# Kernel tuning notes

Hardware: AMD Instinct MI355X
Metric: run time of the kernel (lower is better)

The kernel has to match this reference:

```python
import jax, jax.numpy as jnp
import numpy as np

# Algorithm constants (scaled-down but structure-identical to the source:
# original Nxy=2304, Nz=300, ItN=60, ROISize=300, NxyExt=128, BkgMean=110, SNR=200)
ItN = 2
BkgMean = 110.0
ROISize = 256
SNR = 200.0
NxyExt = 64
Nxy = 1024
Nz = 24
LO = Nxy // 2 - ROISize   # ROI start inside the padded FFT plane
HI = Nxy // 2 + ROISize   # ROI end


def setup_inputs() -> dict:
    key = jax.random.key(0)
    k1, k2, k3, k4 = jax.random.split(key, 4)
    # raw camera image; uniform in [0, 400) so that subtracting BkgMean=110 keeps signal
    imstack = jax.random.uniform(k1, (1, 1, Nxy - 2 * NxyExt, Nxy - 2 * NxyExt), dtype=jnp.float32) * 400.0
    # initial object volume estimate (the `init` ctor arg)
    init_vol = jax.random.uniform(k2, (1, Nz, 2 * ROISize, 2 * ROISize), dtype=jnp.float32)
    # learned frequency-domain PSF kernel (rand * 0.001, as in __init__)
    conv_real = jax.random.uniform(k3, (1, 1, Nxy, Nxy), dtype=jnp.float32) * 0.001
    conv_imag = jax.random.uniform(k4, (1, 1, Nxy, Nxy), dtype=jnp.float32) * 0.001
    return {"imstack": imstack, "init_vol": init_vol, "conv_real": conv_real, "conv_imag": conv_imag}


def reference(imstack, init_vol, conv_real, conv_imag):
    # Complex frequency-domain kernel; constant across iterations (the source
    # rebuilds/casts it every slice -- same math, hoisted here).
    K = (conv_real + 1j * conv_imag)[0, 0]            # [Nxy, Nxy] complex
    Ksum = jnp.sum(conv_real)

    img = jnp.maximum(imstack - BkgMean, 0.0)
    ImgExp = jnp.pad(img, ((0, 0), (0, 0), (NxyExt, NxyExt), (NxyExt, NxyExt)))  # [1,1,Nxy,Nxy]

    obj = init_vol                                     # [1, Nz, 2R, 2R]
    for _ in range(ItN):
        # --- forward projection: batched over all Nz slices (source loops) ---
        # each slice is placed into the center ROI of a zero [Nxy,Nxy] plane
        vol = jnp.pad(obj, ((0, 0), (0, 0), (LO, Nxy - HI), (LO, Nxy - HI)))  # [1,Nz,Nxy,Nxy]
        est = jnp.real(jnp.fft.ifft2(jnp.fft.fft2(vol) * K)) / Ksum
        ImgEst = jnp.sum(jnp.maximum(est, 0.0), axis=1, keepdims=True)        # [1,1,Nxy,Nxy]

        # --- ratio image (interior only; border stays 1) ---
        Tmp = jnp.median(ImgEst)
        inner = ImgExp[:, :, NxyExt:-NxyExt, NxyExt:-NxyExt] / (
            ImgEst[:, :, NxyExt:-NxyExt, NxyExt:-NxyExt] + Tmp / SNR)
        Ratio = jnp.ones((1, 1, Nxy, Nxy), dtype=ImgEst.dtype)
        Ratio = Ratio.at[:, :, NxyExt:-NxyExt, NxyExt:-NxyExt].set(inner)

        # --- back projection: in the source, fft2(Ratio)*conj(K) is identical for
        # every jj (Ratio and K do not change inside the loop), so compute once ---
        back = jnp.real(jnp.fft.ifft2(jnp.fft.fft2(Ratio) * jnp.conj(K))) / Ksum
        back = jnp.maximum(back, 0.0)                  # [1,1,Nxy,Nxy]
        obj = obj * back[:, :, LO:HI, LO:HI]           # broadcast over Nz
    return obj
```

## Files before the change

### kernel.cpp

```cpp
#include <hip/hip_runtime.h>
#include <math.h>

#define NXY  1024
#define NZ   24
#define ROI2 512
#define LO_  256
#define EXT  64
#define IMGW 896
#define ITN  2
#define SNR_ 200.0f
#define BKG  110.0f
#define RANK1 524287u
#define RANK2 524288u
#define NACC 4
#define SWZ(i) ((i) ^ ((((i) >> 4) & 3) * 5))

typedef float2 cf;

__device__ __forceinline__ cf cadd(cf a, cf b) { return make_float2(a.x + b.x, a.y + b.y); }
__device__ __forceinline__ cf csub(cf a, cf b) { return make_float2(a.x - b.x, a.y - b.y); }
__device__ __forceinline__ cf cmul(cf a, cf b) { return make_float2(a.x * b.x - a.y * b.y, a.x * b.y + a.y * b.x); }

struct Tw { const cf *t0, *t1, *t2, *t3; };

__device__ __forceinline__ void twinit_all(cf* TW0, cf* T1, cf* T2, cf* T3) {
  const float W = -6.28318530717958647692f / 1024.0f;
  int k = threadIdx.x;
  float s, c;
  sincosf(W * (float)k, &s, &c);
  TW0[k] = make_float2(c, s);
  if (k < 64) { sincosf(W * (float)(4 * k), &s, &c);  T1[k] = make_float2(c, s); }
  if (k < 16) { sincosf(W * (float)(16 * k), &s, &c); T2[k] = make_float2(c, s); }
  if (k < 4)  { sincosf(W * (float)(64 * k), &s, &c); T3[k] = make_float2(c, s); }
}

template <int SIGN, int T0>
__device__ cf* fft1024_r4_t(cf* src, cf* dst, Tw tw) {
  const int tid = threadIdx.x;
#pragma unroll
  for (int t = T0; t < 5; ++t) {
    __syncthreads();
    const int s = 1 << (2 * t);
    const int q = tid & (s - 1);
    cf a0 = src[SWZ(tid)];
    cf a1 = src[SWZ(tid + 256)];
    cf a2 = src[SWZ(tid + 512)];
    cf a3 = src[SWZ(tid + 768)];
    cf b0 = cadd(a0, a2), b1 = csub(a0, a2);
    cf b2 = cadd(a1, a3), b3 = csub(a1, a3);
    cf jb3 = (SIGN < 0) ? make_float2(b3.y, -b3.x) : make_float2(-b3.y, b3.x);
    cf c0 = cadd(b0, b2);
    cf c2 = csub(b0, b2);
    cf c1 = cadd(b1, jb3);
    cf c3 = csub(b1, jb3);
    const int base = 4 * tid - 3 * q;
    if (t == 4) {
      dst[SWZ(base)]         = c0;
      dst[SWZ(base + s)]     = c1;
      dst[SWZ(base + 2 * s)] = c2;
      dst[SWZ(base + 3 * s)] = c3;
    } else {
      cf t1v = (t == 0) ? tw.t0[tid] : (t == 1) ? tw.t1[tid >> 2]
             : (t == 2) ? tw.t2[tid >> 4] : tw.t3[tid >> 6];
      if (SIGN > 0) t1v.y = -t1v.y;
      cf t2v = cmul(t1v, t1v);
      cf t3v = cmul(t2v, t1v);
      dst[SWZ(base)]         = c0;
      dst[SWZ(base + s)]     = cmul(c1, t1v);
      dst[SWZ(base + 2 * s)] = cmul(c2, t2v);
      dst[SWZ(base + 3 * s)] = cmul(c3, t3v);
    }
    cf* tmp = src; src = dst; dst = tmp;
  }
  __syncthreads();
  return src;
}

__device__ __forceinline__ void fft_stage0_half(cf a1, cf a2, cf* dst, const cf* TW0) {
  const int tid = threadIdx.x;
  cf b1 = make_float2(-a2.x, -a2.y);
  cf jb3 = make_float2(a1.y, -a1.x);
  cf c0 = cadd(a2, a1);
  cf c2 = csub(a2, a1);
  cf c1 = cadd(b1, jb3);
  cf c3 = csub(b1, jb3);
  cf t1v = TW0[tid];
  cf t2v = cmul(t1v, t1v);
  cf t3v = cmul(t2v, t1v);
  const int base = 4 * tid;
  dst[SWZ(base)]     = c0;
  dst[SWZ(base + 1)] = cmul(c1, t1v);
  dst[SWZ(base + 2)] = cmul(c2, t2v);
  dst[SWZ(base + 3)] = cmul(c3, t3v);
}

__global__ void ksum_kernel(const float* __restrict__ a, float* __restrict__ out) {
  __shared__ float s[256];
  int tid = threadIdx.x;
  float acc = 0.f;
  for (int i = blockIdx.x * 256 + tid; i < NXY * NXY; i += gridDim.x * 256) acc += a[i];
  s[tid] = acc;
  __syncthreads();
  for (int o = 128; o > 0; o >>= 1) {
    if (tid < o) s[tid] += s[tid + o];
    __syncthreads();
  }
  if (tid == 0) atomicAdd(out, s[0]);
}

__global__ void imgexp_kernel(const float* __restrict__ im, float* __restrict__ out) {
  int idx = blockIdx.x * 256 + threadIdx.x;
  int r = idx >> 10, c = idx & 1023;
  float v = 0.f;
  if (r >= EXT && r < NXY - EXT && c >= EXT && c < NXY - EXT) {
    float t = im[(size_t)(r - EXT) * IMGW + (c - EXT)] - BKG;
    v = t > 0.f ? t : 0.f;
  }
  out[idx] = v;
}

__global__ void buildkh_kernel(const float* __restrict__ kre, const float* __restrict__ kim,
                               cf* __restrict__ kt) {
  int idx = blockIdx.x * 256 + threadIdx.x;
  if (idx >= 513 * 1024) return;
  int ky = idx & 1023, kx = idx >> 10;
  int ny = (1024 - ky) & 1023, nx = (1024 - kx) & 1023;
  float ar = kre[(size_t)ky * NXY + kx], ai = kim[(size_t)ky * NXY + kx];
  float br = kre[(size_t)ny * NXY + nx], bi = kim[(size_t)ny * NXY + nx];
  kt[idx] = make_float2(0.5f * (ar + br), 0.5f * (ai - bi));
}

__global__ void transpose_kernel(const cf* __restrict__ in, cf* __restrict__ out, int R, int C) {
  __shared__ cf tile[32][33];
  size_t zoff = (size_t)blockIdx.z * R * C;
  const cf* src = in + zoff;
  cf* dst = out + zoff;
  int bc = blockIdx.x * 32, br = blockIdx.y * 32;
  int tx = threadIdx.x, ty = threadIdx.y;
#pragma unroll
  for (int j = 0; j < 32; j += 8) tile[ty + j][tx] = src[(size_t)(br + ty + j) * C + bc + tx];
  __syncthreads();
#pragma unroll
  for (int j = 0; j < 32; j += 8) dst[(size_t)(bc + ty + j) * R + br + tx] = tile[tx][ty + j];
}

__global__ __launch_bounds__(256) void pass1_kernel(const float* __restrict__ in, cf* __restrict__ out) {
  __shared__ cf X[1024], Y[1024], TW0[256], T1[64], T2[16], T3[4];
  int tid = threadIdx.x, b = blockIdx.x, zl = blockIdx.y;
  twinit_all(TW0, T1, T2, T3);
  const float* r0 = in + ((size_t)zl * 512 + 2 * b) * 512;
  const float* r1 = r0 + 512;
  cf a1 = make_float2(r0[tid], r1[tid]);
  cf a2 = make_float2(r0[tid + 256], r1[tid + 256]);
  fft_stage0_half(a1, a2, Y, TW0);
  Tw tw{TW0, T1, T2, T3};
  cf* G = fft1024_r4_t<-1, 1>(Y, X, tw);
  cf* o0 = out + ((size_t)zl * 512 + 2 * b) * 512;
  cf* o1 = o0 + 512;
  for (int k = tid; k < 512; k += 256) {
    if (k == 0) {
      cf g0 = G[SWZ(0)], gn = G[SWZ(512)];
      o0[0] = make_float2(g0.x, gn.x);
      o1[0] = make_float2(g0.y, gn.y);
    } else {
      cf c = G[SWZ(k)], d = G[SWZ(1024 - k)];
      o0[k] = make_float2(0.5f * (c.x + d.x), 0.5f * (c.y - d.y));
      o1[k] = make_float2(0.5f * (c.y + d.y), 0.5f * (d.x - c.x));
    }
  }
}

__global__ __launch_bounds__(256) void pass1b_kernel(const float* __restrict__ iexp,
                                                     const float* __restrict__ iest,
                                                     const float* __restrict__ tos,
                                                     cf* __restrict__ out) {
  __shared__ cf X[1024], Y[1024], TW0[256], T1[64], T2[16], T3[4];
  int tid = threadIdx.x, b = blockIdx.x;
  twinit_all(TW0, T1, T2, T3);
  float t = tos[0];
  int r0 = 2 * b, r1 = 2 * b + 1;
  bool in0 = (r0 >= EXT && r0 < NXY - EXT);
  bool in1 = (r1 >= EXT && r1 < NXY - EXT);
  for (int k = tid; k < 1024; k += 256) {
    bool kin = (k >= EXT && k < NXY - EXT);
    float v0 = (in0 && kin) ? iexp[(size_t)r0 * NXY + k] / (iest[(size_t)r0 * NXY + k] + t) : 1.0f;
    float v1 = (in1 && kin) ? iexp[(size_t)r1 * NXY + k] / (iest[(size_t)r1 * NXY + k] + t) : 1.0f;
    X[SWZ(k)] = make_float2(v0, v1);
  }
  Tw tw{TW0, T1, T2, T3};
  cf* G = fft1024_r4_t<-1, 0>(X, Y, tw);
  cf* o0 = out + (size_t)r0 * 512;
  cf* o1 = out + (size_t)r1 * 512;
  for (int k = tid; k < 512; k += 256) {
    if (k == 0) {
      cf g0 = G[SWZ(0)], gn = G[SWZ(512)];
      o0[0] = make_float2(g0.x, gn.x);
      o1[0] = make_float2(g0.y, gn.y);
    } else {
      cf c = G[SWZ(k)], d = G[SWZ(1024 - k)];
      o0[k] = make_float2(0.5f * (c.x + d.x), 0.5f * (c.y - d.y));
      o1[k] = make_float2(0.5f * (c.y + d.y), 0.5f * (d.x - c.x));
    }
  }
}

template <int HALFIN>
__global__ __launch_bounds__(256) void pass2_kernel(const cf* __restrict__ in,
                                                    const cf* __restrict__ kt, cf* __restrict__ out,
                                                    int zn, int ZB, int conjK) {
  __shared__ cf X[1024], Y[1024], TW0[256], T1[64], T2[16], T3[4];
  int tid = threadIdx.x, kc = blockIdx.x;
  twinit_all(TW0, T1, T2, T3);
  Tw tw{TW0, T1, T2, T3};
  cf kva[4], kvb[4];
#pragma unroll
  for (int j = 0; j < 4; ++j) {
    kva[j] = kt[(size_t)kc * NXY + tid + 256 * j];
    if (conjK) kva[j].y = -kva[j].y;
  }
  if (kc == 0) {
#pragma unroll
    for (int j = 0; j < 4; ++j) {
      kvb[j] = kt[(size_t)512 * NXY + tid + 256 * j];
      if (conjK) kvb[j].y = -kvb[j].y;
    }
  }
  const int inLen = HALFIN ? 512 : 1024;
  int zlo = blockIdx.y * ZB, zhi = min(zn, zlo + ZB);
  for (int z = zlo; z < zhi; ++z) {
    const cf* src = in + ((size_t)z * 512 + kc) * inLen;
    cf* F;
    if (HALFIN) {
      cf a1 = src[tid], a2 = src[tid + 256];
      fft_stage0_half(a1, a2, Y, TW0);
      F = fft1024_r4_t<-1, 1>(Y, X, tw);
    } else {
      for (int k = tid; k < 1024; k += 256) X[SWZ(k)] = src[k];
      F = fft1024_r4_t<-1, 0>(X, Y, tw);
    }
    if (kc == 0) {
      cf fk[4], fn[4];
#pragma unroll
      for (int j = 0; j < 4; ++j) {
        int k = tid + 256 * j, nk = (1024 - k) & 1023;
        fk[j] = F[SWZ(k)];
        fn[j] = F[SWZ(nk)];
      }
      __syncthreads();
#pragma unroll
      for (int j = 0; j < 4; ++j) {
        int k = tid + 256 * j;
        cf Fa = make_float2(0.5f * (fk[j].x + fn[j].x), 0.5f * (fk[j].y - fn[j].y));
        cf Fb = make_float2(0.5f * (fk[j].y + fn[j].y), 0.5f * (fn[j].x - fk[j].x));
        cf Ga = cmul(Fa, kva[j]);
        cf Gb = cmul(Fb, kvb[j]);
        F[SWZ(k)] = make_float2(Ga.x - Gb.y, Ga.y + Gb.x);
      }
    } else {
#pragma unroll
      for (int j = 0; j < 4; ++j) {
        int p = SWZ(tid + 256 * j);
        F[p] = cmul(F[p], kva[j]);
      }
    }
    cf* G = fft1024_r4_t<1, 0>(F, (F == X) ? Y : X, tw);
    cf* dst = out + ((size_t)z * 512 + kc) * NXY;
    for (int k = tid; k < 1024; k += 256) dst[k] = G[SWZ(k)];
  }
}

__global__ __launch_bounds__(256) void pass3_fwd_kernel(const cf* __restrict__ in,
                                                        float* __restrict__ partials,
                                                        const float* __restrict__ ksump, int zn,
                                                        int accum) {
  __shared__ cf X[1024], Y[1024], TW0[256], T1[64], T2[16], T3[4];
  int tid = threadIdx.x, b = blockIdx.x, a = blockIdx.y;
  twinit_all(TW0, T1, T2, T3);
  Tw tw{TW0, T1, T2, T3};
  float scale = 1.0f / (1048576.0f * ksump[0]);
  int r0 = 2 * b, r1 = 2 * b + 1;
  float acc[8] = {0.f, 0.f, 0.f, 0.f, 0.f, 0.f, 0.f, 0.f};
  for (int z = a; z < zn; z += NACC) {
    const cf* s0 = in + ((size_t)z * NXY + r0) * 512;
    const cf* s1 = s0 + 512;
    for (int k = tid; k < 512; k += 256) {
      cf u0 = s0[k], u1 = s1[k];
      if (k == 0) {
        X[SWZ(0)]   = make_float2(u0.x, u1.x);
        X[SWZ(512)] = make_float2(u0.y, u1.y);
      } else {
        X[SWZ(k)]        = make_float2(u0.x - u1.y, u0.y + u1.x);
        X[SWZ(1024 - k)] = make_float2(u0.x + u1.y, u1.x - u0.y);
      }
    }
    cf* G = fft1024_r4_t<1, 0>(X, Y, tw);
#pragma unroll
    for (int j = 0; j < 4; ++j) {
      cf g = G[SWZ(tid + 256 * j)];
      float v0 = g.x * scale, v1 = g.y * scale;
      acc[j]     += v0 > 0.f ? v0 : 0.f;
      acc[4 + j] += v1 > 0.f ? v1 : 0.f;
    }
  }
  float* d0 = partials + ((size_t)a * NXY + r0) * NXY;
  float* d1 = d0 + NXY;
  if (accum) {
#pragma unroll
    for (int j = 0; j < 4; ++j) { d0[tid + 256 * j] += acc[j]; d1[tid + 256 * j] += acc[4 + j]; }
  } else {
#pragma unroll
    for (int j = 0; j < 4; ++j) { d0[tid + 256 * j] = acc[j]; d1[tid + 256 * j] = acc[4 + j]; }
  }
}

__global__ void fold_kernel(const float* __restrict__ partials, float* __restrict__ iest,
                            unsigned* __restrict__ st) {
  int i = blockIdx.x * 256 + threadIdx.x;
  float s = 0.f;
#pragma unroll
  for (int a = 0; a < NACC; ++a) s += partials[(size_t)a * NXY * NXY + i];
  iest[i] = s;
  if (i == 0) { st[0] = 0u; st[1] = 0u; st[2] = RANK1; st[3] = RANK2; }
}

__global__ __launch_bounds__(256) void pass3_back_kernel(const cf* __restrict__ in, float* __restrict__ obj,
                                                         const float* __restrict__ ksump) {
  __shared__ cf X[1024], Y[1024], TW0[256], T1[64], T2[16], T3[4];
  __shared__ float br0[512], br1[512];
  int tid = threadIdx.x, b = blockIdx.x;
  twinit_all(TW0, T1, T2, T3);
  Tw tw{TW0, T1, T2, T3};
  float scale = 1.0f / (1048576.0f * ksump[0]);
  int r0 = LO_ + 2 * b, r1 = r0 + 1;
  const cf* s0 = in + (size_t)r0 * 512;
  const cf* s1 = in + (size_t)r1 * 512;
  for (int k = tid; k < 512; k += 256) {
    cf u0 = s0[k], u1 = s1[k];
    if (k == 0) {
      X[SWZ(0)]   = make_float2(u0.x, u1.x);
      X[SWZ(512)] = make_float2(u0.y, u1.y);
    } else {
      X[SWZ(k)]        = make_float2(u0.x - u1.y, u0.y + u1.x);
      X[SWZ(1024 - k)] = make_float2(u0.x + u1.y, u1.x - u0.y);
    }
  }
  cf* G = fft1024_r4_t<1, 0>(X, Y, tw);
  for (int k = tid; k < 512; k += 256) {
    cf g = G[SWZ(k + LO_)];
    float v0 = g.x * scale, v1 = g.y * scale;
    br0[k] = v0 > 0.f ? v0 : 0.f;
    br1[k] = v1 > 0.f ? v1 : 0.f;
  }
  __syncthreads();
  int rp0 = 2 * b, rp1 = 2 * b + 1;
  for (int idx = tid; idx < NZ * 512; idx += 256) {
    int z = idx >> 9, c = idx & 511;
    obj[((size_t)z * ROI2 + rp0) * ROI2 + c] *= br0[c];
    obj[((size_t)z * ROI2 + rp1) * ROI2 + c] *= br1[c];
  }
}

__global__ void medhist_kernel(const float* __restrict__ v, const unsigned* __restrict__ st,
                               unsigned* __restrict__ hist, int shift, unsigned maskHigh, int nb) {
  extern __shared__ unsigned h[];
  int tid = threadIdx.x;
  for (int k = tid; k < 2 * nb; k += 256) h[k] = 0u;
  __syncthreads();
  unsigned p1 = st[0], p2 = st[1];
  unsigned bm = (unsigned)(nb - 1);
  for (int i = blockIdx.x * 256 + tid; i < NXY * NXY; i += gridDim.x * 256) {
    unsigned u = __float_as_uint(v[i]);
    unsigned b = (u >> shift) & bm;
    if ((u & maskHigh) == (p1 & maskHigh)) atomicAdd(&h[b], 1u);
    if ((u & maskHigh) == (p2 & maskHigh)) atomicAdd(&h[nb + b], 1u);
  }
  __syncthreads();
  for (int k = tid; k < 2 * nb; k += 256) atomicAdd(&hist[k], h[k]);
}

__global__ void medpick_kernel(unsigned* st, const unsigned* __restrict__ hist, int shift, int nb,
                               int finalRound, float* tos) {
  __shared__ unsigned ps[256];
  int t = threadIdx.x;
  int per = nb >> 8;
  for (int which = 0; which < 2; ++which) {
    unsigned loc[8];
    unsigned my = 0;
    for (int i = 0; i < per; ++i) { loc[i] = hist[which * nb + t * per + i]; my += loc[i]; }
    ps[t] = my;
    __syncthreads();
    for (int off = 1; off < 256; off <<= 1) {
      unsigned v = (t >= off) ? ps[t - off] : 0u;
      __syncthreads();
      ps[t] += v;
      __syncthreads();
    }
    unsigned pre = ps[t] - my;
    unsigned r = st[2 + which];
    if (r >= pre && r < pre + my) {
      unsigned cum = pre;
      for (int i = 0; i < per; ++i) {
        if (r < cum + loc[i]) {
          st[which] |= (unsigned)(t * per + i) << shift;
          st[2 + which] = r - cum;
          break;
        }
        cum += loc[i];
      }
    }
    __syncthreads();
  }
  if (finalRound && t == 0) {
    float m = 0.5f * (__uint_as_float(st[0]) + __uint_as_float(st[1]));
    tos[0] = m / SNR_;
  }
}

extern "C" void kernel_launch(void* const* d_in, const int* in_sizes, int n_in,
                              void* d_out, int out_size, void* d_ws, size_t ws_size,
                              hipStream_t stream) {
  const float* imstack  = (const float*)d_in[0];
  const float* init_vol = (const float*)d_in[1];
  const float* conv_re  = (const float*)d_in[2];
  const float* conv_im  = (const float*)d_in[3];
  float* obj = (float*)d_out;

  char* w = (char*)d_ws;
  size_t off = 0;
  auto alloc = [&](size_t bytes) -> void* {
    void* p = (void*)(w + off);
    off += (bytes + 255) & ~(size_t)255;
    return p;
  };

  const size_t PLANE = (size_t)NXY * NXY;
  const size_t HPLANE = (size_t)512 * NXY;
  cf* KT         = (cf*)alloc((size_t)513 * NXY * sizeof(cf));
  float* IExp    = (float*)alloc(PLANE * 4);
  float* IEst    = (float*)alloc(PLANE * 4);
  float* Partial = (float*)alloc((size_t)NACC * PLANE * 4);
  float* Ksum    = (float*)alloc(256);
  unsigned* St   = (unsigned*)alloc(256);
  unsigned* Hist = (unsigned*)alloc(3 * 2 * 2048 * 4);
  size_t fixedEnd = off;

  int ZC = 2;
  const int zcs[7] = {24, 12, 8, 6, 4, 3, 2};
  for (int i = 0; i < 7; ++i) {
    size_t need = fixedEnd + (size_t)zcs[i] * 2ull * HPLANE * sizeof(cf) + 4096;
    if (need <= ws_size) { ZC = zcs[i]; break; }
  }
  cf* bufC = (cf*)alloc((size_t)ZC * HPLANE * sizeof(cf));
  cf* bufD = (cf*)alloc((size_t)ZC * HPLANE * sizeof(cf));
  float* Tos = Ksum + 1;

  hipMemcpyAsync(obj, init_vol, (size_t)NZ * ROI2 * ROI2 * 4, hipMemcpyDeviceToDevice, stream);
  hipMemsetAsync(Ksum, 0, 8, stream);
  ksum_kernel<<<256, 256, 0, stream>>>(conv_re, Ksum);
  imgexp_kernel<<<4096, 256, 0, stream>>>(imstack, IExp);
  buildkh_kernel<<<2052, 256, 0, stream>>>(conv_re, conv_im, KT);

  const int shifts[3] = {21, 10, 0};
  const int nbs[3]    = {2048, 2048, 1024};
  const unsigned masks[3] = {0u, 0xFFE00000u, 0xFFFFFC00u};

  for (int it = 0; it < ITN; ++it) {
    for (int z0 = 0; z0 < NZ; z0 += ZC) {
      int zn = (NZ - z0 < ZC) ? (NZ - z0) : ZC;
      int nzb = (zn + 5) / 6;
      pass1_kernel<<<dim3(256, zn), 256, 0, stream>>>(obj + (size_t)z0 * ROI2 * ROI2, bufC);
      transpose_kernel<<<dim3(16, 16, zn), dim3(32, 8), 0, stream>>>(bufC, bufD, 512, 512);
      pass2_kernel<1><<<dim3(512, nzb), 256, 0, stream>>>(bufD, KT, bufC, zn, 6, 0);
      transpose_kernel<<<dim3(32, 16, zn), dim3(32, 8), 0, stream>>>(bufC, bufD, 512, 1024);
      pass3_fwd_kernel<<<dim3(512, NACC), 256, 0, stream>>>(bufD, Partial, Ksum, zn, z0 > 0 ? 1 : 0);
    }
    fold_kernel<<<4096, 256, 0, stream>>>(Partial, IEst, St);
    hipMemsetAsync(Hist, 0, 3 * 2 * 2048 * 4, stream);
    for (int round = 0; round < 3; ++round) {
      medhist_kernel<<<256, 256, 2 * nbs[round] * 4, stream>>>(IEst, St, Hist + round * 4096,
                                                               shifts[round], masks[round], nbs[round]);
      medpick_kernel<<<1, 256, 0, stream>>>(St, Hist + round * 4096, shifts[round], nbs[round],
                                            round == 2 ? 1 : 0, Tos);
    }
    pass1b_kernel<<<512, 256, 0, stream>>>(IExp, IEst, Tos, bufC);
    transpose_kernel<<<dim3(16, 32, 1), dim3(32, 8), 0, stream>>>(bufC, bufD, 1024, 512);
    pass2_kernel<0><<<dim3(512, 1), 256, 0, stream>>>(bufD, KT, bufC, 1, 1, 1);
    transpose_kernel<<<dim3(32, 16, 1), dim3(32, 8), 0, stream>>>(bufC, bufD, 512, 1024);
    pass3_back_kernel<<<256, 256, 0, stream>>>(bufD, obj, Ksum);
  }
}
```

Measured before the change: 632.8 us.

## Replace block-wide radix-4 FFT with per-wavefront register radix-16 FFT

```diff
diff --git a/kernel.cpp b/kernel.cpp
--- a/kernel.cpp
+++ b/kernel.cpp
@@ -13,7 +13,7 @@
 #define RANK1 524287u
 #define RANK2 524288u
 #define NACC 4
-#define SWZ(i) ((i) ^ ((((i) >> 4) & 3) * 5))
+#define LSWZ(i) ((i) ^ (((i) >> 4) & 15))
 
 typedef float2 cf;
 
@@ -21,77 +21,82 @@
 __device__ __forceinline__ cf csub(cf a, cf b) { return make_float2(a.x - b.x, a.y - b.y); }
 __device__ __forceinline__ cf cmul(cf a, cf b) { return make_float2(a.x * b.x - a.y * b.y, a.x * b.y + a.y * b.x); }
 
-struct Tw { const cf *t0, *t1, *t2, *t3; };
-
-__device__ __forceinline__ void twinit_all(cf* TW0, cf* T1, cf* T2, cf* T3) {
-  const float W = -6.28318530717958647692f / 1024.0f;
-  int k = threadIdx.x;
-  float s, c;
-  sincosf(W * (float)k, &s, &c);
-  TW0[k] = make_float2(c, s);
-  if (k < 64) { sincosf(W * (float)(4 * k), &s, &c);  T1[k] = make_float2(c, s); }
-  if (k < 16) { sincosf(W * (float)(16 * k), &s, &c); T2[k] = make_float2(c, s); }
-  if (k < 4)  { sincosf(W * (float)(64 * k), &s, &c); T3[k] = make_float2(c, s); }
-}
-
-template <int SIGN, int T0>
-__device__ cf* fft1024_r4_t(cf* src, cf* dst, Tw tw) {
-  const int tid = threadIdx.x;
-#pragma unroll
-  for (int t = T0; t < 5; ++t) {
-    __syncthreads();
-    const int s = 1 << (2 * t);
-    const int q = tid & (s - 1);
-    cf a0 = src[SWZ(tid)];
-    cf a1 = src[SWZ(tid + 256)];
-    cf a2 = src[SWZ(tid + 512)];
-    cf a3 = src[SWZ(tid + 768)];
-    cf b0 = cadd(a0, a2), b1 = csub(a0, a2);
-    cf b2 = cadd(a1, a3), b3 = csub(a1, a3);
-    cf jb3 = (SIGN < 0) ? make_float2(b3.y, -b3.x) : make_float2(-b3.y, b3.x);
-    cf c0 = cadd(b0, b2);
-    cf c2 = csub(b0, b2);
-    cf c1 = cadd(b1, jb3);
-    cf c3 = csub(b1, jb3);
-    const int base = 4 * tid - 3 * q;
-    if (t == 4) {
-      dst[SWZ(base)]         = c0;
-      dst[SWZ(base + s)]     = c1;
-      dst[SWZ(base + 2 * s)] = c2;
-      dst[SWZ(base + 3 * s)] = c3;
-    } else {
-      cf t1v = (t == 0) ? tw.t0[tid] : (t == 1) ? tw.t1[tid >> 2]
-             : (t == 2) ? tw.t2[tid >> 4] : tw.t3[tid >> 6];
-      if (SIGN > 0) t1v.y = -t1v.y;
-      cf t2v = cmul(t1v, t1v);
-      cf t3v = cmul(t2v, t1v);
-      dst[SWZ(base)]         = c0;
-      dst[SWZ(base + s)]     = cmul(c1, t1v);
-      dst[SWZ(base + 2 * s)] = cmul(c2, t2v);
-      dst[SWZ(base + 3 * s)] = cmul(c3, t3v);
-    }
-    cf* tmp = src; src = dst; dst = tmp;
-  }
-  __syncthreads();
-  return src;
-}
-
-__device__ __forceinline__ void fft_stage0_half(cf a1, cf a2, cf* dst, const cf* TW0) {
-  const int tid = threadIdx.x;
-  cf b1 = make_float2(-a2.x, -a2.y);
-  cf jb3 = make_float2(a1.y, -a1.x);
-  cf c0 = cadd(a2, a1);
-  cf c2 = csub(a2, a1);
-  cf c1 = cadd(b1, jb3);
-  cf c3 = csub(b1, jb3);
-  cf t1v = TW0[tid];
-  cf t2v = cmul(t1v, t1v);
-  cf t3v = cmul(t2v, t1v);
-  const int base = 4 * tid;
-  dst[SWZ(base)]     = c0;
-  dst[SWZ(base + 1)] = cmul(c1, t1v);
-  dst[SWZ(base + 2)] = cmul(c2, t2v);
-  dst[SWZ(base + 3)] = cmul(c3, t3v);
+template <int SIGN>
+__device__ __forceinline__ cf wc(float cr, float ci) { return make_float2(cr, SIGN < 0 ? ci : -ci); }
+
+template <int SIGN>
+__device__ __forceinline__ void dft4r(cf& a0, cf& a1, cf& a2, cf& a3) {
+  cf b0 = cadd(a0, a2), b1 = csub(a0, a2);
+  cf b2 = cadd(a1, a3), b3 = csub(a1, a3);
+  cf jb3 = (SIGN < 0) ? make_float2(b3.y, -b3.x) : make_float2(-b3.y, b3.x);
+  a0 = cadd(b0, b2); a2 = csub(b0, b2);
+  a1 = cadd(b1, jb3); a3 = csub(b1, jb3);
+}
+
+template <int SIGN>
+__device__ __forceinline__ void dft16r(cf* x) {
+  const cf W1 = wc<SIGN>(0.92387953251f, -0.38268343236f);
+  const cf W2 = wc<SIGN>(0.70710678119f, -0.70710678119f);
+  const cf W3 = wc<SIGN>(0.38268343236f, -0.92387953251f);
+  const cf W4 = wc<SIGN>(0.f, -1.f);
+  const cf W6 = wc<SIGN>(-0.70710678119f, -0.70710678119f);
+  const cf W9 = wc<SIGN>(-0.92387953251f, 0.38268343236f);
+  cf t[16];
+#pragma unroll
+  for (int p = 0; p < 4; ++p) {
+    cf a0 = x[p], a1 = x[p + 4], a2 = x[p + 8], a3 = x[p + 12];
+    dft4r<SIGN>(a0, a1, a2, a3);
+    if (p == 1) { a1 = cmul(a1, W1); a2 = cmul(a2, W2); a3 = cmul(a3, W3); }
+    else if (p == 2) { a1 = cmul(a1, W2); a2 = cmul(a2, W4); a3 = cmul(a3, W6); }
+    else if (p == 3) { a1 = cmul(a1, W3); a2 = cmul(a2, W6); a3 = cmul(a3, W9); }
+    t[4 * p] = a0; t[4 * p + 1] = a1; t[4 * p + 2] = a2; t[4 * p + 3] = a3;
+  }
+#pragma unroll
+  for (int q = 0; q < 4; ++q) {
+    cf a0 = t[q], a1 = t[q + 4], a2 = t[q + 8], a3 = t[q + 12];
+    dft4r<SIGN>(a0, a1, a2, a3);
+    x[q] = a0; x[q + 4] = a1; x[q + 8] = a2; x[q + 12] = a3;
+  }
+}
+
+__device__ __forceinline__ void twpow(cf* w, cf w1) {
+  w[0] = make_float2(1.f, 0.f);
+  w[1] = w1;
+  w[2] = cmul(w1, w1);   w[3] = cmul(w[2], w1);
+  w[4] = cmul(w[2], w[2]); w[5] = cmul(w[3], w[2]);
+  w[6] = cmul(w[3], w[3]); w[7] = cmul(w[4], w[3]);
+  w[8] = cmul(w[4], w[4]); w[9] = cmul(w[5], w[4]);
+  w[10] = cmul(w[5], w[5]); w[11] = cmul(w[6], w[5]);
+  w[12] = cmul(w[6], w[6]); w[13] = cmul(w[7], w[6]);
+  w[14] = cmul(w[7], w[7]); w[15] = cmul(w[8], w[7]);
+}
+
+template <int SIGN>
+__device__ void fft1024_wave(cf* r, cf* L, int lane) {
+  const float TH = (SIGN < 0) ? -6.28318530717958647692f : 6.28318530717958647692f;
+  cf w[16];
+  float sv, cv;
+  dft16r<SIGN>(r);
+  sincosf(TH * (float)lane * (1.0f / 1024.0f), &sv, &cv);
+  twpow(w, make_float2(cv, sv));
+#pragma unroll
+  for (int m = 1; m < 16; ++m) r[m] = cmul(r[m], w[m]);
+#pragma unroll
+  for (int m = 0; m < 16; ++m) L[LSWZ(16 * lane + m)] = r[m];
+#pragma unroll
+  for (int m = 0; m < 16; ++m) r[m] = L[LSWZ(lane + 64 * m)];
+  dft16r<SIGN>(r);
+  int p1 = lane >> 4, q1 = lane & 15;
+  sincosf(TH * (float)p1 * (1.0f / 64.0f), &sv, &cv);
+  twpow(w, make_float2(cv, sv));
+#pragma unroll
+  for (int m = 1; m < 16; ++m) r[m] = cmul(r[m], w[m]);
+#pragma unroll
+  for (int m = 0; m < 16; ++m) L[LSWZ(q1 + 256 * p1 + 16 * m)] = r[m];
+#pragma unroll
+  for (int j = 0; j < 16; ++j) r[j] = L[LSWZ(lane + 64 * j)];
+#pragma unroll
+  for (int a = 0; a < 4; ++a) dft4r<SIGN>(r[a], r[a + 4], r[a + 8], r[a + 12]);
 }
 
 __global__ void ksum_kernel(const float* __restrict__ a, float* __restrict__ out) {
@@ -145,25 +150,34 @@
 }
 
 __global__ __launch_bounds__(256) void pass1_kernel(const float* __restrict__ in, cf* __restrict__ out) {
-  __shared__ cf X[1024], Y[1024], TW0[256], T1[64], T2[16], T3[4];
-  int tid = threadIdx.x, b = blockIdx.x, zl = blockIdx.y;
-  twinit_all(TW0, T1, T2, T3);
-  const float* r0 = in + ((size_t)zl * 512 + 2 * b) * 512;
+  __shared__ cf Lb[4][1024];
+  int tid = threadIdx.x, wid = tid >> 6, lane = tid & 63;
+  cf* L = Lb[wid];
+  int b = blockIdx.x * 4 + wid, z = blockIdx.y;
+  const float* r0 = in + ((size_t)z * 512 + 2 * b) * 512;
   const float* r1 = r0 + 512;
-  cf a1 = make_float2(r0[tid], r1[tid]);
-  cf a2 = make_float2(r0[tid + 256], r1[tid + 256]);
-  fft_stage0_half(a1, a2, Y, TW0);
-  Tw tw{TW0, T1, T2, T3};
-  cf* G = fft1024_r4_t<-1, 1>(Y, X, tw);
-  cf* o0 = out + ((size_t)zl * 512 + 2 * b) * 512;
+  cf r[16];
+#pragma unroll
+  for (int m = 0; m < 16; ++m) r[m] = make_float2(0.f, 0.f);
+#pragma unroll
+  for (int m = 4; m < 12; ++m) {
+    int idx = lane + 64 * m - 256;
+    r[m] = make_float2(r0[idx], r1[idx]);
+  }
+  fft1024_wave<-1>(r, L, lane);
+#pragma unroll
+  for (int j = 0; j < 16; ++j) L[LSWZ(lane + 64 * j)] = r[j];
+  cf* o0 = out + ((size_t)z * 512 + 2 * b) * 512;
   cf* o1 = o0 + 512;
-  for (int k = tid; k < 512; k += 256) {
+#pragma unroll
+  for (int j = 0; j < 8; ++j) {
+    int k = lane + 64 * j;
+    int nk = k ? (1024 - k) : 512;
+    cf c = L[LSWZ(k)], d = L[LSWZ(nk)];
     if (k == 0) {
-      cf g0 = G[SWZ(0)], gn = G[SWZ(512)];
-      o0[0] = make_float2(g0.x, gn.x);
-      o1[0] = make_float2(g0.y, gn.y);
+      o0[0] = make_float2(c.x, d.x);
+      o1[0] = make_float2(c.y, d.y);
     } else {
-      cf c = G[SWZ(k)], d = G[SWZ(1024 - k)];
       o0[k] = make_float2(0.5f * (c.x + d.x), 0.5f * (c.y - d.y));
       o1[k] = make_float2(0.5f * (c.y + d.y), 0.5f * (d.x - c.x));
     }
@@ -174,30 +188,37 @@
                                                      const float* __restrict__ iest,
                                                      const float* __restrict__ tos,
                                                      cf* __restrict__ out) {
-  __shared__ cf X[1024], Y[1024], TW0[256], T1[64], T2[16], T3[4];
-  int tid = threadIdx.x, b = blockIdx.x;
-  twinit_all(TW0, T1, T2, T3);
+  __shared__ cf Lb[4][1024];
+  int tid = threadIdx.x, wid = tid >> 6, lane = tid & 63;
+  cf* L = Lb[wid];
+  int b = blockIdx.x * 4 + wid;
   float t = tos[0];
   int r0 = 2 * b, r1 = 2 * b + 1;
   bool in0 = (r0 >= EXT && r0 < NXY - EXT);
   bool in1 = (r1 >= EXT && r1 < NXY - EXT);
-  for (int k = tid; k < 1024; k += 256) {
+  cf r[16];
+#pragma unroll
+  for (int m = 0; m < 16; ++m) {
+    int k = lane + 64 * m;
     bool kin = (k >= EXT && k < NXY - EXT);
     float v0 = (in0 && kin) ? iexp[(size_t)r0 * NXY + k] / (iest[(size_t)r0 * NXY + k] + t) : 1.0f;
     float v1 = (in1 && kin) ? iexp[(size_t)r1 * NXY + k] / (iest[(size_t)r1 * NXY + k] + t) : 1.0f;
-    X[SWZ(k)] = make_float2(v0, v1);
-  }
-  Tw tw{TW0, T1, T2, T3};
-  cf* G = fft1024_r4_t<-1, 0>(X, Y, tw);
+    r[m] = make_float2(v0, v1);
+  }
+  fft1024_wave<-1>(r, L, lane);
+#pragma unroll
+  for (int j = 0; j < 16; ++j) L[LSWZ(lane + 64 * j)] = r[j];
   cf* o0 = out + (size_t)r0 * 512;
   cf* o1 = out + (size_t)r1 * 512;
-  for (int k = tid; k < 512; k += 256) {
+#pragma unroll
+  for (int j = 0; j < 8; ++j) {
+    int k = lane + 64 * j;
+    int nk = k ? (1024 - k) : 512;
+    cf c = L[LSWZ(k)], d = L[LSWZ(nk)];
     if (k == 0) {
-      cf g0 = G[SWZ(0)], gn = G[SWZ(512)];
-      o0[0] = make_float2(g0.x, gn.x);
-      o1[0] = make_float2(g0.y, gn.y);
+      o0[0] = make_float2(c.x, d.x);
+      o1[0] = make_float2(c.y, d.y);
     } else {
-      cf c = G[SWZ(k)], d = G[SWZ(1024 - k)];
       o0[k] = make_float2(0.5f * (c.x + d.x), 0.5f * (c.y - d.y));
       o1[k] = make_float2(0.5f * (c.y + d.y), 0.5f * (d.x - c.x));
     }
@@ -207,109 +228,103 @@
 template <int HALFIN>
 __global__ __launch_bounds__(256) void pass2_kernel(const cf* __restrict__ in,
                                                     const cf* __restrict__ kt, cf* __restrict__ out,
-                                                    int zn, int ZB, int conjK) {
-  __shared__ cf X[1024], Y[1024], TW0[256], T1[64], T2[16], T3[4];
-  int tid = threadIdx.x, kc = blockIdx.x;
-  twinit_all(TW0, T1, T2, T3);
-  Tw tw{TW0, T1, T2, T3};
-  cf kva[4], kvb[4];
-#pragma unroll
-  for (int j = 0; j < 4; ++j) {
-    kva[j] = kt[(size_t)kc * NXY + tid + 256 * j];
+                                                    int conjK) {
+  __shared__ cf Lb[4][1024];
+  int tid = threadIdx.x, wid = tid >> 6, lane = tid & 63;
+  cf* L = Lb[wid];
+  int kc = blockIdx.x * 4 + wid, z = blockIdx.y;
+  cf kva[16];
+#pragma unroll
+  for (int j = 0; j < 16; ++j) {
+    kva[j] = kt[(size_t)kc * NXY + lane + 64 * j];
     if (conjK) kva[j].y = -kva[j].y;
   }
+  const int inLen = HALFIN ? 512 : 1024;
+  const cf* src = in + ((size_t)z * 512 + kc) * inLen;
+  cf r[16];
+  if (HALFIN) {
+#pragma unroll
+    for (int m = 0; m < 16; ++m) r[m] = make_float2(0.f, 0.f);
+#pragma unroll
+    for (int m = 4; m < 12; ++m) r[m] = src[lane + 64 * m - 256];
+  } else {
+#pragma unroll
+    for (int m = 0; m < 16; ++m) r[m] = src[lane + 64 * m];
+  }
+  fft1024_wave<-1>(r, L, lane);
   if (kc == 0) {
 #pragma unroll
-    for (int j = 0; j < 4; ++j) {
-      kvb[j] = kt[(size_t)512 * NXY + tid + 256 * j];
-      if (conjK) kvb[j].y = -kvb[j].y;
-    }
-  }
-  const int inLen = HALFIN ? 512 : 1024;
-  int zlo = blockIdx.y * ZB, zhi = min(zn, zlo + ZB);
-  for (int z = zlo; z < zhi; ++z) {
-    const cf* src = in + ((size_t)z * 512 + kc) * inLen;
-    cf* F;
-    if (HALFIN) {
-      cf a1 = src[tid], a2 = src[tid + 256];
-      fft_stage0_half(a1, a2, Y, TW0);
-      F = fft1024_r4_t<-1, 1>(Y, X, tw);
-    } else {
-      for (int k = tid; k < 1024; k += 256) X[SWZ(k)] = src[k];
-      F = fft1024_r4_t<-1, 0>(X, Y, tw);
-    }
-    if (kc == 0) {
-      cf fk[4], fn[4];
-#pragma unroll
-      for (int j = 0; j < 4; ++j) {
-        int k = tid + 256 * j, nk = (1024 - k) & 1023;
-        fk[j] = F[SWZ(k)];
-        fn[j] = F[SWZ(nk)];
-      }
-      __syncthreads();
-#pragma unroll
-      for (int j = 0; j < 4; ++j) {
-        int k = tid + 256 * j;
-        cf Fa = make_float2(0.5f * (fk[j].x + fn[j].x), 0.5f * (fk[j].y - fn[j].y));
-        cf Fb = make_float2(0.5f * (fk[j].y + fn[j].y), 0.5f * (fn[j].x - fk[j].x));
-        cf Ga = cmul(Fa, kva[j]);
-        cf Gb = cmul(Fb, kvb[j]);
-        F[SWZ(k)] = make_float2(Ga.x - Gb.y, Ga.y + Gb.x);
-      }
-    } else {
-#pragma unroll
-      for (int j = 0; j < 4; ++j) {
-        int p = SWZ(tid + 256 * j);
-        F[p] = cmul(F[p], kva[j]);
-      }
-    }
-    cf* G = fft1024_r4_t<1, 0>(F, (F == X) ? Y : X, tw);
-    cf* dst = out + ((size_t)z * 512 + kc) * NXY;
-    for (int k = tid; k < 1024; k += 256) dst[k] = G[SWZ(k)];
-  }
+    for (int j = 0; j < 16; ++j) L[LSWZ(lane + 64 * j)] = r[j];
+#pragma unroll
+    for (int j = 0; j < 16; ++j) {
+      int k = lane + 64 * j;
+      int nk = (1024 - k) & 1023;
+      cf c = L[LSWZ(k)], d = L[LSWZ(nk)];
+      cf Fa = make_float2(0.5f * (c.x + d.x), 0.5f * (c.y - d.y));
+      cf Fb = make_float2(0.5f * (c.y + d.y), 0.5f * (d.x - c.x));
+      cf kb = kt[(size_t)512 * NXY + k];
+      if (conjK) kb.y = -kb.y;
+      cf Ga = cmul(Fa, kva[j]);
+      cf Gb = cmul(Fb, kb);
+      r[j] = make_float2(Ga.x - Gb.y, Ga.y + Gb.x);
+    }
+  } else {
+#pragma unroll
+    for (int j = 0; j < 16; ++j) r[j] = cmul(r[j], kva[j]);
+  }
+  fft1024_wave<1>(r, L, lane);
+  cf* dst = out + ((size_t)z * 512 + kc) * NXY;
+#pragma unroll
+  for (int j = 0; j < 16; ++j) dst[lane + 64 * j] = r[j];
 }
 
 __global__ __launch_bounds__(256) void pass3_fwd_kernel(const cf* __restrict__ in,
                                                         float* __restrict__ partials,
                                                         const float* __restrict__ ksump, int zn,
                                                         int accum) {
-  __shared__ cf X[1024], Y[1024], TW0[256], T1[64], T2[16], T3[4];
-  int tid = threadIdx.x, b = blockIdx.x, a = blockIdx.y;
-  twinit_all(TW0, T1, T2, T3);
-  Tw tw{TW0, T1, T2, T3};
+  __shared__ cf Lb[4][1024];
+  int tid = threadIdx.x, wid = tid >> 6, lane = tid & 63;
+  cf* L = Lb[wid];
+  int b = blockIdx.x * 4 + wid, a = blockIdx.y;
   float scale = 1.0f / (1048576.0f * ksump[0]);
   int r0 = 2 * b, r1 = 2 * b + 1;
-  float acc[8] = {0.f, 0.f, 0.f, 0.f, 0.f, 0.f, 0.f, 0.f};
+  cf acc[16];
+#pragma unroll
+  for (int j = 0; j < 16; ++j) acc[j] = make_float2(0.f, 0.f);
+  cf r[16];
   for (int z = a; z < zn; z += NACC) {
     const cf* s0 = in + ((size_t)z * NXY + r0) * 512;
     const cf* s1 = s0 + 512;
-    for (int k = tid; k < 512; k += 256) {
+#pragma unroll
+    for (int j = 0; j < 8; ++j) {
+      int k = lane + 64 * j;
       cf u0 = s0[k], u1 = s1[k];
       if (k == 0) {
-        X[SWZ(0)]   = make_float2(u0.x, u1.x);
-        X[SWZ(512)] = make_float2(u0.y, u1.y);
+        L[LSWZ(0)]   = make_float2(u0.x, u1.x);
+        L[LSWZ(512)] = make_float2(u0.y, u1.y);
       } else {
-        X[SWZ(k)]        = make_float2(u0.x - u1.y, u0.y + u1.x);
-        X[SWZ(1024 - k)] = make_float2(u0.x + u1.y, u1.x - u0.y);
+        L[LSWZ(k)]        = make_float2(u0.x - u1.y, u0.y + u1.x);
+        L[LSWZ(1024 - k)] = make_float2(u0.x + u1.y, u1.x - u0.y);
       }
     }
-    cf* G = fft1024_r4_t<1, 0>(X, Y, tw);
-#pragma unroll
-    for (int j = 0; j < 4; ++j) {
-      cf g = G[SWZ(tid + 256 * j)];
-      float v0 = g.x * scale, v1 = g.y * scale;
-      acc[j]     += v0 > 0.f ? v0 : 0.f;
-      acc[4 + j] += v1 > 0.f ? v1 : 0.f;
+#pragma unroll
+    for (int m = 0; m < 16; ++m) r[m] = L[LSWZ(lane + 64 * m)];
+    fft1024_wave<1>(r, L, lane);
+#pragma unroll
+    for (int j = 0; j < 16; ++j) {
+      float v0 = r[j].x * scale, v1 = r[j].y * scale;
+      acc[j].x += v0 > 0.f ? v0 : 0.f;
+      acc[j].y += v1 > 0.f ? v1 : 0.f;
     }
   }
   float* d0 = partials + ((size_t)a * NXY + r0) * NXY;
   float* d1 = d0 + NXY;
   if (accum) {
 #pragma unroll
-    for (int j = 0; j < 4; ++j) { d0[tid + 256 * j] += acc[j]; d1[tid + 256 * j] += acc[4 + j]; }
+    for (int j = 0; j < 16; ++j) { d0[lane + 64 * j] += acc[j].x; d1[lane + 64 * j] += acc[j].y; }
   } else {
 #pragma unroll
-    for (int j = 0; j < 4; ++j) { d0[tid + 256 * j] = acc[j]; d1[tid + 256 * j] = acc[4 + j]; }
+    for (int j = 0; j < 16; ++j) { d0[lane + 64 * j] = acc[j].x; d1[lane + 64 * j] = acc[j].y; }
   }
 }
 
@@ -325,44 +340,51 @@
 
 __global__ __launch_bounds__(256) void pass3_back_kernel(const cf* __restrict__ in, float* __restrict__ obj,
                                                          const float* __restrict__ ksump) {
-  __shared__ cf X[1024], Y[1024], TW0[256], T1[64], T2[16], T3[4];
-  __shared__ float br0[512], br1[512];
-  int tid = threadIdx.x, b = blockIdx.x;
-  twinit_all(TW0, T1, T2, T3);
-  Tw tw{TW0, T1, T2, T3};
+  __shared__ cf Lb[4][1024];
+  int tid = threadIdx.x, wid = tid >> 6, lane = tid & 63;
+  cf* L = Lb[wid];
+  int b = blockIdx.x * 4 + wid;
   float scale = 1.0f / (1048576.0f * ksump[0]);
   int r0 = LO_ + 2 * b, r1 = r0 + 1;
   const cf* s0 = in + (size_t)r0 * 512;
   const cf* s1 = in + (size_t)r1 * 512;
-  for (int k = tid; k < 512; k += 256) {
+#pragma unroll
+  for (int j = 0; j < 8; ++j) {
+    int k = lane + 64 * j;
     cf u0 = s0[k], u1 = s1[k];
     if (k == 0) {
-      X[SWZ(0)]   = make_float2(u0.x, u1.x);
-      X[SWZ(512)] = make_float2(u0.y, u1.y);
+      L[LSWZ(0)]   = make_float2(u0.x, u1.x);
+      L[LSWZ(512)] = make_float2(u0.y, u1.y);
     } else {
-      X[SWZ(k)]        = make_float2(u0.x - u1.y, u0.y + u1.x);
-      X[SWZ(1024 - k)] = make_float2(u0.x + u1.y, u1.x - u0.y);
-    }
-  }
-  cf* G = fft1024_r4_t<1, 0>(X, Y, tw);
-  for (int k = tid; k < 512; k += 256) {
-    cf g = G[SWZ(k + LO_)];
-    float v0 = g.x * scale, v1 = g.y * scale;
-    br0[k] = v0 > 0.f ? v0 : 0.f;
-    br1[k] = v1 > 0.f ? v1 : 0.f;
-  }
-  __syncthreads();
+      L[LSWZ(k)]        = make_float2(u0.x - u1.y, u0.y + u1.x);
+      L[LSWZ(1024 - k)] = make_float2(u0.x + u1.y, u1.x - u0.y);
+    }
+  }
+  cf r[16];
+#pragma unroll
+  for (int m = 0; m < 16; ++m) r[m] = L[LSWZ(lane + 64 * m)];
+  fft1024_wave<1>(r, L, lane);
+#pragma unroll
+  for (int j = 4; j < 12; ++j) {
+    int c = lane + 64 * j - 256;
+    float v0 = r[j].x * scale, v1 = r[j].y * scale;
+    L[c] = make_float2(v0 > 0.f ? v0 : 0.f, v1 > 0.f ? v1 : 0.f);
+  }
   int rp0 = 2 * b, rp1 = 2 * b + 1;
-  for (int idx = tid; idx < NZ * 512; idx += 256) {
+  for (int idx = lane; idx < NZ * 512; idx += 64) {
     int z = idx >> 9, c = idx & 511;
-    obj[((size_t)z * ROI2 + rp0) * ROI2 + c] *= br0[c];
-    obj[((size_t)z * ROI2 + rp1) * ROI2 + c] *= br1[c];
-  }
-}
-
-__global__ void medhist_kernel(const float* __restrict__ v, const unsigned* __restrict__ st,
-                               unsigned* __restrict__ hist, int shift, unsigned maskHigh, int nb) {
+    cf br = L[c];
+    obj[((size_t)z * ROI2 + rp0) * ROI2 + c] *= br.x;
+    obj[((size_t)z * ROI2 + rp1) * ROI2 + c] *= br.y;
+  }
+}
+
+__global__ void medhist_kernel(const float* __restrict__ v, unsigned* __restrict__ st,
+                               unsigned* __restrict__ hist, int shift, unsigned maskHigh, int nb,
+                               int finalRound, float* __restrict__ tos) {
   extern __shared__ unsigned h[];
+  __shared__ unsigned ps[256];
+  __shared__ int lastFlag;
   int tid = threadIdx.x;
   for (int k = tid; k < 2 * nb; k += 256) h[k] = 0u;
   __syncthreads();
@@ -376,33 +398,34 @@
   }
   __syncthreads();
   for (int k = tid; k < 2 * nb; k += 256) atomicAdd(&hist[k], h[k]);
-}
-
-__global__ void medpick_kernel(unsigned* st, const unsigned* __restrict__ hist, int shift, int nb,
-                               int finalRound, float* tos) {
-  __shared__ unsigned ps[256];
-  int t = threadIdx.x;
+  __syncthreads();
+  if (tid == 0) {
+    __threadfence();
+    lastFlag = (atomicAdd(&hist[4096], 1u) == (unsigned)(gridDim.x - 1)) ? 1 : 0;
+  }
+  __syncthreads();
+  if (!lastFlag) return;
   int per = nb >> 8;
   for (int which = 0; which < 2; ++which) {
     unsigned loc[8];
     unsigned my = 0;
-    for (int i = 0; i < per; ++i) { loc[i] = hist[which * nb + t * per + i]; my += loc[i]; }
-    ps[t] = my;
+    for (int i = 0; i < per; ++i) { loc[i] = atomicAdd(&hist[which * nb + tid * per + i], 0u); my += loc[i]; }
+    ps[tid] = my;
     __syncthreads();
     for (int off = 1; off < 256; off <<= 1) {
-      unsigned v = (t >= off) ? ps[t - off] : 0u;
+      unsigned vv = (tid >= off) ? ps[tid - off] : 0u;
       __syncthreads();
-      ps[t] += v;
+      ps[tid] += vv;
       __syncthreads();
     }
-    unsigned pre = ps[t] - my;
-    unsigned r = st[2 + which];
-    if (r >= pre && r < pre + my) {
+    unsigned pre = ps[tid] - my;
+    unsigned rr = st[2 + which];
+    if (rr >= pre && rr < pre + my) {
       unsigned cum = pre;
       for (int i = 0; i < per; ++i) {
-        if (r < cum + loc[i]) {
-          st[which] |= (unsigned)(t * per + i) << shift;
-          st[2 + which] = r - cum;
+        if (rr < cum + loc[i]) {
+          st[which] |= (unsigned)(tid * per + i) << shift;
+          st[2 + which] = rr - cum;
           break;
         }
         cum += loc[i];
@@ -410,7 +433,7 @@
     }
     __syncthreads();
   }
-  if (finalRound && t == 0) {
+  if (finalRound && tid == 0) {
     float m = 0.5f * (__uint_as_float(st[0]) + __uint_as_float(st[1]));
     tos[0] = m / SNR_;
   }
@@ -441,7 +464,7 @@
   float* Partial = (float*)alloc((size_t)NACC * PLANE * 4);
   float* Ksum    = (float*)alloc(256);
   unsigned* St   = (unsigned*)alloc(256);
-  unsigned* Hist = (unsigned*)alloc(3 * 2 * 2048 * 4);
+  unsigned* Hist = (unsigned*)alloc(3 * 4160 * 4);
   size_t fixedEnd = off;
 
   int ZC = 2;
@@ -467,25 +490,23 @@
   for (int it = 0; it < ITN; ++it) {
     for (int z0 = 0; z0 < NZ; z0 += ZC) {
       int zn = (NZ - z0 < ZC) ? (NZ - z0) : ZC;
-      int nzb = (zn + 5) / 6;
-      pass1_kernel<<<dim3(256, zn), 256, 0, stream>>>(obj + (size_t)z0 * ROI2 * ROI2, bufC);
+      pass1_kernel<<<dim3(64, zn), 256, 0, stream>>>(obj + (size_t)z0 * ROI2 * ROI2, bufC);
       transpose_kernel<<<dim3(16, 16, zn), dim3(32, 8), 0, stream>>>(bufC, bufD, 512, 512);
-      pass2_kernel<1><<<dim3(512, nzb), 256, 0, stream>>>(bufD, KT, bufC, zn, 6, 0);
+      pass2_kernel<1><<<dim3(128, zn), 256, 0, stream>>>(bufD, KT, bufC, 0);
       transpose_kernel<<<dim3(32, 16, zn), dim3(32, 8), 0, stream>>>(bufC, bufD, 512, 1024);
-      pass3_fwd_kernel<<<dim3(512, NACC), 256, 0, stream>>>(bufD, Partial, Ksum, zn, z0 > 0 ? 1 : 0);
+      pass3_fwd_kernel<<<dim3(128, NACC), 256, 0, stream>>>(bufD, Partial, Ksum, zn, z0 > 0 ? 1 : 0);
     }
     fold_kernel<<<4096, 256, 0, stream>>>(Partial, IEst, St);
-    hipMemsetAsync(Hist, 0, 3 * 2 * 2048 * 4, stream);
+    hipMemsetAsync(Hist, 0, 3 * 4160 * 4, stream);
     for (int round = 0; round < 3; ++round) {
-      medhist_kernel<<<256, 256, 2 * nbs[round] * 4, stream>>>(IEst, St, Hist + round * 4096,
-                                                               shifts[round], masks[round], nbs[round]);
-      medpick_kernel<<<1, 256, 0, stream>>>(St, Hist + round * 4096, shifts[round], nbs[round],
-                                            round == 2 ? 1 : 0, Tos);
-    }
-    pass1b_kernel<<<512, 256, 0, stream>>>(IExp, IEst, Tos, bufC);
+      medhist_kernel<<<256, 256, 2 * nbs[round] * 4, stream>>>(IEst, St, Hist + round * 4160,
+                                                               shifts[round], masks[round], nbs[round],
+                                                               round == 2 ? 1 : 0, Tos);
+    }
+    pass1b_kernel<<<128, 256, 0, stream>>>(IExp, IEst, Tos, bufC);
     transpose_kernel<<<dim3(16, 32, 1), dim3(32, 8), 0, stream>>>(bufC, bufD, 1024, 512);
-    pass2_kernel<0><<<dim3(512, 1), 256, 0, stream>>>(bufD, KT, bufC, 1, 1, 1);
+    pass2_kernel<0><<<dim3(128, 1), 256, 0, stream>>>(bufD, KT, bufC, 1);
     transpose_kernel<<<dim3(32, 16, 1), dim3(32, 8), 0, stream>>>(bufC, bufD, 512, 1024);
-    pass3_back_kernel<<<256, 256, 0, stream>>>(bufD, obj, Ksum);
-  }
-}
+    pass3_back_kernel<<<64, 256, 0, stream>>>(bufD, obj, Ksum);
+  }
+}
```

Result: slower. 742.1 us (+17.3%).
